# Kernel tuning notes

Measured on AMD Instinct MI355X. Metric: run time of the kernel, lower is better.

Reference implementation:

```python
import jax, jax.numpy as jnp
import numpy as np

ALPHA = 0.25
GAMMA = 2.0
CLS_EPS = 1e-4


def _make_boxes(key, n, img=512.0, smin=32.0, smax=128.0, yx=False):
    k1, k2, k3, k4 = jax.random.split(key, 4)
    cx = jax.random.uniform(k1, (n,)) * img
    cy = jax.random.uniform(k2, (n,)) * img
    w = smin + jax.random.uniform(k3, (n,)) * (smax - smin)
    h = smin + jax.random.uniform(k4, (n,)) * (smax - smin)
    if yx:  # anchor format (y1, x1, y2, x2)
        return jnp.stack([cy - h / 2, cx - w / 2, cy + h / 2, cx + w / 2], axis=1)
    # annotation format (x1, y1, x2, y2)
    return jnp.stack([cx - w / 2, cy - h / 2, cx + w / 2, cy + h / 2], axis=1)


def setup_inputs() -> dict:
    key = jax.random.key(0)
    B, A, C, M = 4, 100000, 80, 32
    k = jax.random.split(key, 6)
    classifications = jax.random.uniform(k[0], (B, A, C), dtype=jnp.float32)
    regressions = jax.random.normal(k[1], (B, A, 7), dtype=jnp.float32)
    anchors = _make_boxes(k[2], A, yx=True)[None]  # [1, A, 4] (y1,x1,y2,x2)
    boxes = jax.vmap(lambda kk: _make_boxes(kk, M))(jax.random.split(k[3], B))  # [B, M, 4]
    labels = jax.random.randint(k[4], (B, M), 0, C).astype(jnp.float32)
    annotations = jnp.concatenate([boxes, labels[..., None]], axis=-1)  # [B, M, 5]
    return {"classifications": classifications, "regressions": regressions,
            "anchors": anchors, "annotations": annotations}


def reference(classifications, regressions, anchors, annotations):
    B, A, C = classifications.shape
    anchor = anchors[0]  # [A, 4] (y1, x1, y2, x2)
    aw = anchor[:, 3] - anchor[:, 1]
    ah = anchor[:, 2] - anchor[:, 0]
    acx = anchor[:, 1] + 0.5 * aw
    acy = anchor[:, 0] + 0.5 * ah
    area_a = (anchor[:, 2] - anchor[:, 0]) * (anchor[:, 3] - anchor[:, 1])

    def per_image(cls, reg, ann):
        M_ = ann.shape[0]
        b = ann[:, :4]  # (x1, y1, x2, y2)
        labels = ann[:, 4].astype(jnp.int32)
        cls = jnp.clip(cls, CLS_EPS, 1.0 - CLS_EPS)
        # IoU [A, M] (same axis convention as calc_iou)
        iw = jnp.clip(jnp.minimum(anchor[:, 3:4], b[None, :, 2]) - jnp.maximum(anchor[:, 1:2], b[None, :, 0]), 0.0)
        ih = jnp.clip(jnp.minimum(anchor[:, 2:3], b[None, :, 3]) - jnp.maximum(anchor[:, 0:1], b[None, :, 1]), 0.0)
        area_b = (b[:, 2] - b[:, 0]) * (b[:, 3] - b[:, 1])
        inter = iw * ih
        ua = jnp.clip(area_a[:, None] + area_b[None, :] - inter, 1e-8)
        iou = inter / ua
        iou_max = iou.max(axis=1)
        iou_argmax = iou.argmax(axis=1)  # [A]
        pos = iou_max >= 0.5
        neg = iou_max < 0.4
        num_pos = pos.sum()
        posf = pos.astype(cls.dtype)
        # classification targets: -1 ignore, 0 background, one-hot positives
        assigned_box = b[iou_argmax]           # [A, 4]
        assigned_lbl = labels[iou_argmax]      # [A]
        onehot = jax.nn.one_hot(assigned_lbl, C, dtype=cls.dtype)
        tgt = jnp.where(pos[:, None], onehot, jnp.where(neg[:, None], 0.0, -1.0))
        alpha_f = jnp.where(tgt == 1.0, ALPHA, 1.0 - ALPHA)
        focal_w = alpha_f * jnp.where(tgt == 1.0, 1.0 - cls, cls) ** GAMMA
        bce = -(tgt * jnp.log(cls) + (1.0 - tgt) * jnp.log(1.0 - cls))
        cls_loss = jnp.where(tgt != -1.0, focal_w * bce, 0.0).sum() / jnp.maximum(num_pos.astype(cls.dtype), 1.0)
        gw = assigned_box[:, 2] - assigned_box[:, 0]
        gh = assigned_box[:, 3] - assigned_box[:, 1]
        gcx = assigned_box[:, 0] + 0.5 * gw
        gcy = assigned_box[:, 1] + 0.5 * gh
        gw = jnp.clip(gw, 1.0)
        gh = jnp.clip(gh, 1.0)
        rt = jnp.stack([(gcy - acy) / ah, (gcx - acx) / aw,
                        jnp.log(gh / ah), jnp.log(gw / aw)], axis=1)  # [A, 4] (dy,dx,dh,dw)
        diff = jnp.abs(rt - reg[:, :4])
        sl1 = jnp.where(diff <= 1.0 / 9.0, 0.5 * 9.0 * diff ** 2, diff - 0.5 / 9.0)
        reg_loss = (sl1 * posf[:, None]).sum() / jnp.maximum(num_pos * 4, 1).astype(cls.dtype)
        # embedding grouping loss (segment mean per GT box over positive anchors)
        emb = reg[:, 4:7]
        counts = jax.ops.segment_sum(posf, iou_argmax, num_segments=M_)          # [M]
        sums = jax.ops.segment_sum(emb * posf[:, None], iou_argmax, num_segments=M_)  # [M, 3]
        mean = jnp.where((counts > 0)[:, None], sums / jnp.maximum(counts, 1.0)[:, None], 0.0)
        mdet = jax.lax.stop_gradient(mean)
        sq = jax.ops.segment_sum((((emb - mdet[iou_argmax]) ** 2).sum(-1)) * posf, iou_argmax, num_segments=M_)
        per_ann = jnp.where(counts > 0, sq / jnp.maximum(counts * 3.0, 1.0), 0.0)
        emb_loss = per_ann.sum() / M_
        return cls_loss, reg_loss, emb_loss, mean

    cls_l, reg_l, emb_l, embs = jax.vmap(per_image)(classifications, regressions, annotations)
    losses = jnp.stack([cls_l.mean(), reg_l.mean() * 50.0, emb_l.mean()])
    return losses, embs
```

## Files before the change

### kernel.cpp

```cpp
#include <hip/hip_runtime.h>

#define ALPHA 0.25f
#define CLS_LO 1.0e-4f
#define CLS_HI 0.9999f


__device__ __forceinline__ float smooth_l1(float d) {
    d = fabsf(d);
    return (d <= (1.0f / 9.0f)) ? (4.5f * d * d) : (d - (0.5f / 9.0f));
}

__device__ __forceinline__ float neg_focal(float p) {
    return 0.75f * p * p * (-__logf(1.0f - p));
}

__global__ void __launch_bounds__(256)
det_main_kernel(const float* __restrict__ cls,
                const float* __restrict__ reg,
                const float* __restrict__ anc,
                const float* __restrict__ ann,
                float* __restrict__ ws,
                int A, int C, int M)
{
    const int b   = blockIdx.y;
    const int tid = threadIdx.x;
    const int a0  = blockIdx.x * 256;
    const int a   = a0 + tid;
    const int wsStride = 5 * M + 3;

    __shared__ float sb[5 * 64];
    __shared__ float s_cnt[64], s_sx[64], s_sy[64], s_sz[64], s_sq[64];
    __shared__ float s_scal[3];
    __shared__ float s_maskf[256];

    for (int i = tid; i < M * 5; i += 256)
        sb[i] = ann[(size_t)b * M * 5 + i];
    if (tid < M) { s_cnt[tid] = 0.f; s_sx[tid] = 0.f; s_sy[tid] = 0.f; s_sz[tid] = 0.f; s_sq[tid] = 0.f; }
    if (tid < 3) s_scal[tid] = 0.f;
    s_maskf[tid] = 0.f;
    __syncthreads();

    float contrib_cls = 0.f, contrib_reg = 0.f, contrib_np = 0.f;

    if (a < A) {
        float4 av = ((const float4*)anc)[a];
        const float ay1 = av.x, ax1 = av.y, ay2 = av.z, ax2 = av.w;
        const float aw  = ax2 - ax1;
        const float ah  = ay2 - ay1;
        const float acx = ax1 + 0.5f * aw;
        const float acy = ay1 + 0.5f * ah;
        const float area_a = ah * aw;

        float best = -1.0f;
        int   bj   = 0;
        for (int j = 0; j < M; j++) {
            const float bx1 = sb[j * 5 + 0];
            const float by1 = sb[j * 5 + 1];
            const float bx2 = sb[j * 5 + 2];
            const float by2 = sb[j * 5 + 3];
            float iw = fminf(ax2, bx2) - fmaxf(ax1, bx1); iw = fmaxf(iw, 0.f);
            float ih = fminf(ay2, by2) - fmaxf(ay1, by1); ih = fmaxf(ih, 0.f);
            const float inter = iw * ih;
            const float ua = fmaxf(area_a + (bx2 - bx1) * (by2 - by1) - inter, 1e-8f);
            const float iou = inter / ua;
            if (iou > best) { best = iou; bj = j; }
        }
        const bool pos = best >= 0.5f;
        const bool neg = best < 0.4f;
        s_maskf[tid] = (pos || neg) ? 1.0f : 0.0f;

        if (pos) {
            contrib_np = 1.0f;

            const float* cbase = cls + ((size_t)b * A + a) * (size_t)C;
            const int L = (int)sb[bj * 5 + 4];
            const float p = fminf(fmaxf(cbase[L], CLS_LO), CLS_HI);
            contrib_cls = 0.25f * (1.f - p) * (1.f - p) * (-__logf(p)) - neg_focal(p);

            const float* rp = reg + ((size_t)b * A + a) * 7;
            const float r0 = rp[0], r1 = rp[1], r2 = rp[2], r3 = rp[3];
            const float e0 = rp[4], e1 = rp[5], e2 = rp[6];

            const float bx1 = sb[bj * 5 + 0];
            const float by1 = sb[bj * 5 + 1];
            const float bx2 = sb[bj * 5 + 2];
            const float by2 = sb[bj * 5 + 3];
            float gw = bx2 - bx1;
            float gh = by2 - by1;
            const float gcx = bx1 + 0.5f * gw;
            const float gcy = by1 + 0.5f * gh;
            gw = fmaxf(gw, 1.f);
            gh = fmaxf(gh, 1.f);
            const float t0 = (gcy - acy) / ah;
            const float t1 = (gcx - acx) / aw;
            const float t2 = logf(gh / ah);
            const float t3 = logf(gw / aw);
            contrib_reg = smooth_l1(t0 - r0) + smooth_l1(t1 - r1) +
                          smooth_l1(t2 - r2) + smooth_l1(t3 - r3);

            atomicAdd(&s_cnt[bj], 1.f);
            atomicAdd(&s_sx[bj], e0);
            atomicAdd(&s_sy[bj], e1);
            atomicAdd(&s_sz[bj], e2);
            atomicAdd(&s_sq[bj], e0 * e0 + e1 * e1 + e2 * e2);
        }
    }
    __syncthreads();

    {
        const int nA = min(256, A - a0);
        const int n_elem = nA * C;
        const float4* tile = (const float4*)(cls + ((size_t)b * A + a0) * (size_t)C);
        float acc = 0.f;
        for (int e4 = tid; e4 * 4 < n_elem; e4 += 256) {
            const float4 v = tile[e4];
            const unsigned e = (unsigned)(e4 * 4);
            const unsigned i0 = (e * 52429u) >> 22;
            const unsigned i1 = ((e + 1u) * 52429u) >> 22;
            const unsigned i2 = ((e + 2u) * 52429u) >> 22;
            const unsigned i3 = ((e + 3u) * 52429u) >> 22;
            float p;
            p = fminf(fmaxf(v.x, CLS_LO), CLS_HI); acc += s_maskf[i0] * neg_focal(p);
            p = fminf(fmaxf(v.y, CLS_LO), CLS_HI); acc += s_maskf[i1] * neg_focal(p);
            p = fminf(fmaxf(v.z, CLS_LO), CLS_HI); acc += s_maskf[i2] * neg_focal(p);
            p = fminf(fmaxf(v.w, CLS_LO), CLS_HI); acc += s_maskf[i3] * neg_focal(p);
        }
        contrib_cls += acc;
    }

    for (int off = 32; off > 0; off >>= 1) {
        contrib_cls += __shfl_down(contrib_cls, off, 64);
        contrib_reg += __shfl_down(contrib_reg, off, 64);
        contrib_np  += __shfl_down(contrib_np,  off, 64);
    }
    if ((tid & 63) == 0) {
        atomicAdd(&s_scal[0], contrib_cls);
        atomicAdd(&s_scal[1], contrib_reg);
        atomicAdd(&s_scal[2], contrib_np);
    }
    __syncthreads();

    float* wsb = ws + (size_t)b * wsStride;
    if (tid < M) {
        const float c = s_cnt[tid];
        if (c != 0.f) {
            atomicAdd(&wsb[tid], c);
            atomicAdd(&wsb[M + 3 * tid + 0], s_sx[tid]);
            atomicAdd(&wsb[M + 3 * tid + 1], s_sy[tid]);
            atomicAdd(&wsb[M + 3 * tid + 2], s_sz[tid]);
            atomicAdd(&wsb[4 * M + tid], s_sq[tid]);
        }
    }
    if (tid == 0) {
        atomicAdd(&wsb[5 * M + 0], s_scal[0]);
        atomicAdd(&wsb[5 * M + 1], s_scal[1]);
        atomicAdd(&wsb[5 * M + 2], s_scal[2]);
    }
}

__global__ void det_final_kernel(const float* __restrict__ ws,
                                 float* __restrict__ out,
                                 int B, int M)
{
    const int t = threadIdx.x;
    const int wsStride = 5 * M + 3;
    __shared__ float s_emb[8];
    if (t < B) s_emb[t] = 0.f;
    __syncthreads();

    if (t < B * M) {
        const int b = t / M;
        const int m = t - b * M;
        const float* wsb = ws + (size_t)b * wsStride;
        const float c = wsb[m];
        float mx = 0.f, my = 0.f, mz = 0.f, pa = 0.f;
        if (c > 0.f) {
            mx = wsb[M + 3 * m + 0] / c;
            my = wsb[M + 3 * m + 1] / c;
            mz = wsb[M + 3 * m + 2] / c;
            const float sq = wsb[4 * M + m] - c * (mx * mx + my * my + mz * mz);
            pa = sq / fmaxf(c * 3.f, 1.f);
        }
        out[3 + (size_t)(b * M + m) * 3 + 0] = mx;
        out[3 + (size_t)(b * M + m) * 3 + 1] = my;
        out[3 + (size_t)(b * M + m) * 3 + 2] = mz;
        atomicAdd(&s_emb[b], pa);
    }
    __syncthreads();

    if (t == 0) {
        float cl = 0.f, rl = 0.f, el = 0.f;
        for (int b = 0; b < B; b++) {
            const float* wsb = ws + (size_t)b * wsStride;
            const float np = wsb[5 * M + 2];
            cl += wsb[5 * M + 0] / fmaxf(np, 1.f);
            rl += wsb[5 * M + 1] / fmaxf(4.f * np, 1.f);
            el += s_emb[b] / (float)M;
        }
        const float invB = 1.f / (float)B;
        out[0] = cl * invB;
        out[1] = rl * invB * 50.f;
        out[2] = el * invB;
    }
}

extern "C" void kernel_launch(void* const* d_in, const int* in_sizes, int n_in,
                              void* d_out, int out_size, void* d_ws, size_t ws_size,
                              hipStream_t stream) {
    const float* cls = (const float*)d_in[0];
    const float* reg = (const float*)d_in[1];
    const float* anc = (const float*)d_in[2];
    const float* ann = (const float*)d_in[3];
    float* out = (float*)d_out;
    float* ws  = (float*)d_ws;

    const int A = in_sizes[2] / 4;
    const int B = in_sizes[1] / (A * 7);
    const int C = in_sizes[0] / (B * A);
    const int M = in_sizes[3] / (B * 5);
    const int wsStride = 5 * M + 3;

    hipMemsetAsync(ws, 0, (size_t)B * wsStride * sizeof(float), stream);

    dim3 grid((A + 255) / 256, B);
    det_main_kernel<<<grid, 256, 0, stream>>>(cls, reg, anc, ann, ws, A, C, M);
    det_final_kernel<<<1, 256, 0, stream>>>(ws, out, B, M);
}
```

Baseline: 235.1 us.

## Unroll IoU loop, streamline negative focal pass, replace global atomics with per-block slots

Unrolls the 32-box IoU argmax loop when M is 32. Specialises the dense negative-focal streaming loop for full tiles with C=80, using one mask lookup per float4, FMA accumulation and the 0.75 factor hoisted out. Per-block scalar sums go to dedicated workspace slots instead of global atomics, and the final kernel reduces them. This aims to cut integer index math, ALU work and atomic contention, at the cost of a larger workspace and a serial per-image reduction in the single-block final kernel.

```diff
diff --git a/kernel.cpp b/kernel.cpp
--- a/kernel.cpp
+++ b/kernel.cpp
@@ -1,6 +1,5 @@
 #include <hip/hip_runtime.h>
 
-#define ALPHA 0.25f
 #define CLS_LO 1.0e-4f
 #define CLS_HI 0.9999f
 
@@ -8,10 +7,6 @@
 __device__ __forceinline__ float smooth_l1(float d) {
     d = fabsf(d);
     return (d <= (1.0f / 9.0f)) ? (4.5f * d * d) : (d - (0.5f / 9.0f));
-}
-
-__device__ __forceinline__ float neg_focal(float p) {
-    return 0.75f * p * p * (-__logf(1.0f - p));
 }
 
 __global__ void __launch_bounds__(256)
@@ -20,23 +15,21 @@
                 const float* __restrict__ anc,
                 const float* __restrict__ ann,
                 float* __restrict__ ws,
-                int A, int C, int M)
+                int A, int C, int M, int NB)
 {
     const int b   = blockIdx.y;
     const int tid = threadIdx.x;
     const int a0  = blockIdx.x * 256;
     const int a   = a0 + tid;
-    const int wsStride = 5 * M + 3;
+    const int S   = 5 * M + 3 * NB;
 
     __shared__ float sb[5 * 64];
     __shared__ float s_cnt[64], s_sx[64], s_sy[64], s_sz[64], s_sq[64];
-    __shared__ float s_scal[3];
     __shared__ float s_maskf[256];
 
     for (int i = tid; i < M * 5; i += 256)
         sb[i] = ann[(size_t)b * M * 5 + i];
     if (tid < M) { s_cnt[tid] = 0.f; s_sx[tid] = 0.f; s_sy[tid] = 0.f; s_sz[tid] = 0.f; s_sq[tid] = 0.f; }
-    if (tid < 3) s_scal[tid] = 0.f;
     s_maskf[tid] = 0.f;
     __syncthreads();
 
@@ -53,18 +46,27 @@
 
         float best = -1.0f;
         int   bj   = 0;
-        for (int j = 0; j < M; j++) {
-            const float bx1 = sb[j * 5 + 0];
-            const float by1 = sb[j * 5 + 1];
-            const float bx2 = sb[j * 5 + 2];
-            const float by2 = sb[j * 5 + 3];
-            float iw = fminf(ax2, bx2) - fmaxf(ax1, bx1); iw = fmaxf(iw, 0.f);
-            float ih = fminf(ay2, by2) - fmaxf(ay1, by1); ih = fmaxf(ih, 0.f);
-            const float inter = iw * ih;
-            const float ua = fmaxf(area_a + (bx2 - bx1) * (by2 - by1) - inter, 1e-8f);
-            const float iou = inter / ua;
-            if (iou > best) { best = iou; bj = j; }
-        }
+#define IOU_BODY(j)                                                              \
+        {                                                                        \
+            const float bx1 = sb[(j) * 5 + 0];                                   \
+            const float by1 = sb[(j) * 5 + 1];                                   \
+            const float bx2 = sb[(j) * 5 + 2];                                   \
+            const float by2 = sb[(j) * 5 + 3];                                   \
+            float iw = fminf(ax2, bx2) - fmaxf(ax1, bx1); iw = fmaxf(iw, 0.f);   \
+            float ih = fminf(ay2, by2) - fmaxf(ay1, by1); ih = fmaxf(ih, 0.f);   \
+            const float inter = iw * ih;                                         \
+            const float ua = fmaxf(area_a + (bx2 - bx1) * (by2 - by1) - inter,   \
+                                   1e-8f);                                       \
+            const float iou = inter / ua;                                        \
+            if (iou > best) { best = iou; bj = (j); }                            \
+        }
+        if (M == 32) {
+            #pragma unroll
+            for (int j = 0; j < 32; j++) IOU_BODY(j)
+        } else {
+            for (int j = 0; j < M; j++) IOU_BODY(j)
+        }
+#undef IOU_BODY
         const bool pos = best >= 0.5f;
         const bool neg = best < 0.4f;
         s_maskf[tid] = (pos || neg) ? 1.0f : 0.0f;
@@ -75,7 +77,8 @@
             const float* cbase = cls + ((size_t)b * A + a) * (size_t)C;
             const int L = (int)sb[bj * 5 + 4];
             const float p = fminf(fmaxf(cbase[L], CLS_LO), CLS_HI);
-            contrib_cls = 0.25f * (1.f - p) * (1.f - p) * (-__logf(p)) - neg_focal(p);
+            contrib_cls = 0.25f * (1.f - p) * (1.f - p) * (-__logf(p))
+                        - 0.75f * p * p * (-__logf(1.f - p));
 
             const float* rp = reg + ((size_t)b * A + a) * 7;
             const float r0 = rp[0], r1 = rp[1], r2 = rp[2], r3 = rp[3];
@@ -91,12 +94,10 @@
             const float gcy = by1 + 0.5f * gh;
             gw = fmaxf(gw, 1.f);
             gh = fmaxf(gh, 1.f);
-            const float t0 = (gcy - acy) / ah;
-            const float t1 = (gcx - acx) / aw;
-            const float t2 = logf(gh / ah);
-            const float t3 = logf(gw / aw);
-            contrib_reg = smooth_l1(t0 - r0) + smooth_l1(t1 - r1) +
-                          smooth_l1(t2 - r2) + smooth_l1(t3 - r3);
+            contrib_reg = smooth_l1((gcy - acy) / ah - r0) +
+                          smooth_l1((gcx - acx) / aw - r1) +
+                          smooth_l1(logf(gh / ah) - r2) +
+                          smooth_l1(logf(gw / aw) - r3);
 
             atomicAdd(&s_cnt[bj], 1.f);
             atomicAdd(&s_sx[bj], e0);
@@ -108,24 +109,37 @@
     __syncthreads();
 
     {
-        const int nA = min(256, A - a0);
-        const int n_elem = nA * C;
         const float4* tile = (const float4*)(cls + ((size_t)b * A + a0) * (size_t)C);
         float acc = 0.f;
-        for (int e4 = tid; e4 * 4 < n_elem; e4 += 256) {
-            const float4 v = tile[e4];
-            const unsigned e = (unsigned)(e4 * 4);
-            const unsigned i0 = (e * 52429u) >> 22;
-            const unsigned i1 = ((e + 1u) * 52429u) >> 22;
-            const unsigned i2 = ((e + 2u) * 52429u) >> 22;
-            const unsigned i3 = ((e + 3u) * 52429u) >> 22;
-            float p;
-            p = fminf(fmaxf(v.x, CLS_LO), CLS_HI); acc += s_maskf[i0] * neg_focal(p);
-            p = fminf(fmaxf(v.y, CLS_LO), CLS_HI); acc += s_maskf[i1] * neg_focal(p);
-            p = fminf(fmaxf(v.z, CLS_LO), CLS_HI); acc += s_maskf[i2] * neg_focal(p);
-            p = fminf(fmaxf(v.w, CLS_LO), CLS_HI); acc += s_maskf[i3] * neg_focal(p);
-        }
-        contrib_cls += acc;
+        if (a0 + 256 <= A && C == 80) {
+            #pragma unroll 5
+            for (int k = 0; k < 20; k++) {
+                const int e4 = tid + 256 * k;
+                const float m = s_maskf[(unsigned)e4 / 20u];
+                const float4 v = tile[e4];
+                float p, l, s = 0.f;
+                p = fminf(fmaxf(v.x, CLS_LO), CLS_HI); l = __logf(1.f - p); s = fmaf(p * p, l, s);
+                p = fminf(fmaxf(v.y, CLS_LO), CLS_HI); l = __logf(1.f - p); s = fmaf(p * p, l, s);
+                p = fminf(fmaxf(v.z, CLS_LO), CLS_HI); l = __logf(1.f - p); s = fmaf(p * p, l, s);
+                p = fminf(fmaxf(v.w, CLS_LO), CLS_HI); l = __logf(1.f - p); s = fmaf(p * p, l, s);
+                acc = fmaf(m, s, acc);
+            }
+        } else {
+            const int nA   = min(256, A - a0);
+            const int cpa4 = C >> 2;
+            const int n4   = nA * cpa4;
+            for (int e4 = tid; e4 < n4; e4 += 256) {
+                const float m = s_maskf[(unsigned)e4 / (unsigned)cpa4];
+                const float4 v = tile[e4];
+                float p, l, s = 0.f;
+                p = fminf(fmaxf(v.x, CLS_LO), CLS_HI); l = __logf(1.f - p); s = fmaf(p * p, l, s);
+                p = fminf(fmaxf(v.y, CLS_LO), CLS_HI); l = __logf(1.f - p); s = fmaf(p * p, l, s);
+                p = fminf(fmaxf(v.z, CLS_LO), CLS_HI); l = __logf(1.f - p); s = fmaf(p * p, l, s);
+                p = fminf(fmaxf(v.w, CLS_LO), CLS_HI); l = __logf(1.f - p); s = fmaf(p * p, l, s);
+                acc = fmaf(m, s, acc);
+            }
+        }
+        contrib_cls -= 0.75f * acc;
     }
 
     for (int off = 32; off > 0; off >>= 1) {
@@ -133,14 +147,15 @@
         contrib_reg += __shfl_down(contrib_reg, off, 64);
         contrib_np  += __shfl_down(contrib_np,  off, 64);
     }
+    __shared__ float s_part[4][3];
     if ((tid & 63) == 0) {
-        atomicAdd(&s_scal[0], contrib_cls);
-        atomicAdd(&s_scal[1], contrib_reg);
-        atomicAdd(&s_scal[2], contrib_np);
-    }
-    __syncthreads();
-
-    float* wsb = ws + (size_t)b * wsStride;
+        s_part[tid >> 6][0] = contrib_cls;
+        s_part[tid >> 6][1] = contrib_reg;
+        s_part[tid >> 6][2] = contrib_np;
+    }
+    __syncthreads();
+
+    float* wsb = ws + (size_t)b * S;
     if (tid < M) {
         const float c = s_cnt[tid];
         if (c != 0.f) {
@@ -152,26 +167,52 @@
         }
     }
     if (tid == 0) {
-        atomicAdd(&wsb[5 * M + 0], s_scal[0]);
-        atomicAdd(&wsb[5 * M + 1], s_scal[1]);
-        atomicAdd(&wsb[5 * M + 2], s_scal[2]);
-    }
-}
-
-__global__ void det_final_kernel(const float* __restrict__ ws,
-                                 float* __restrict__ out,
-                                 int B, int M)
+        float* slot = wsb + 5 * M + 3 * blockIdx.x;
+        slot[0] = s_part[0][0] + s_part[1][0] + s_part[2][0] + s_part[3][0];
+        slot[1] = s_part[0][1] + s_part[1][1] + s_part[2][1] + s_part[3][1];
+        slot[2] = s_part[0][2] + s_part[1][2] + s_part[2][2] + s_part[3][2];
+    }
+}
+
+__global__ void __launch_bounds__(256)
+det_final_kernel(const float* __restrict__ ws,
+                 float* __restrict__ out,
+                 int B, int M, int NB)
 {
     const int t = threadIdx.x;
-    const int wsStride = 5 * M + 3;
+    const int S = 5 * M + 3 * NB;
+    __shared__ float s_scal[8][3];
     __shared__ float s_emb[8];
+    __shared__ float tmp[4][3];
     if (t < B) s_emb[t] = 0.f;
-    __syncthreads();
+
+    for (int b = 0; b < B; b++) {
+        const float* slots = ws + (size_t)b * S + 5 * M;
+        float c = 0.f, r = 0.f, n = 0.f;
+        for (int i = t; i < NB; i += 256) {
+            c += slots[3 * i + 0];
+            r += slots[3 * i + 1];
+            n += slots[3 * i + 2];
+        }
+        for (int off = 32; off > 0; off >>= 1) {
+            c += __shfl_down(c, off, 64);
+            r += __shfl_down(r, off, 64);
+            n += __shfl_down(n, off, 64);
+        }
+        if ((t & 63) == 0) { tmp[t >> 6][0] = c; tmp[t >> 6][1] = r; tmp[t >> 6][2] = n; }
+        __syncthreads();
+        if (t == 0) {
+            s_scal[b][0] = tmp[0][0] + tmp[1][0] + tmp[2][0] + tmp[3][0];
+            s_scal[b][1] = tmp[0][1] + tmp[1][1] + tmp[2][1] + tmp[3][1];
+            s_scal[b][2] = tmp[0][2] + tmp[1][2] + tmp[2][2] + tmp[3][2];
+        }
+        __syncthreads();
+    }
 
     if (t < B * M) {
         const int b = t / M;
         const int m = t - b * M;
-        const float* wsb = ws + (size_t)b * wsStride;
+        const float* wsb = ws + (size_t)b * S;
         const float c = wsb[m];
         float mx = 0.f, my = 0.f, mz = 0.f, pa = 0.f;
         if (c > 0.f) {
@@ -191,10 +232,9 @@
     if (t == 0) {
         float cl = 0.f, rl = 0.f, el = 0.f;
         for (int b = 0; b < B; b++) {
-            const float* wsb = ws + (size_t)b * wsStride;
-            const float np = wsb[5 * M + 2];
-            cl += wsb[5 * M + 0] / fmaxf(np, 1.f);
-            rl += wsb[5 * M + 1] / fmaxf(4.f * np, 1.f);
+            const float np = s_scal[b][2];
+            cl += s_scal[b][0] / fmaxf(np, 1.f);
+            rl += s_scal[b][1] / fmaxf(4.f * np, 1.f);
             el += s_emb[b] / (float)M;
         }
         const float invB = 1.f / (float)B;
@@ -218,11 +258,12 @@
     const int B = in_sizes[1] / (A * 7);
     const int C = in_sizes[0] / (B * A);
     const int M = in_sizes[3] / (B * 5);
-    const int wsStride = 5 * M + 3;
-
-    hipMemsetAsync(ws, 0, (size_t)B * wsStride * sizeof(float), stream);
-
-    dim3 grid((A + 255) / 256, B);
-    det_main_kernel<<<grid, 256, 0, stream>>>(cls, reg, anc, ann, ws, A, C, M);
-    det_final_kernel<<<1, 256, 0, stream>>>(ws, out, B, M);
-}
+    const int NB = (A + 255) / 256;
+    const int S  = 5 * M + 3 * NB;
+
+    hipMemsetAsync(ws, 0, (size_t)B * S * sizeof(float), stream);
+
+    dim3 grid(NB, B);
+    det_main_kernel<<<grid, 256, 0, stream>>>(cls, reg, anc, ann, ws, A, C, M, NB);
+    det_final_kernel<<<1, 256, 0, stream>>>(ws, out, B, M, NB);
+}
```

After: 224.9 us. 1.05x faster.
